# Kernel optimization log

Hardware: AMD Instinct MI355X
Metric: run time of the kernel (lower is better)

Reference implementation:

```python
import jax, jax.numpy as jnp
import numpy as np
from jax import lax

VOCAB, EMB, HID, B, T = 512, 128, 64, 256, 1024

def setup_inputs() -> dict:
    key = jax.random.key(0)
    ks = jax.random.split(key, 16)
    s = 0.1  # small init to keep tanh in its linear-ish range
    return {
        'x': jax.random.randint(ks[0], (B, T), 0, VOCAB),
        'emb': jax.random.normal(ks[1], (VOCAB, EMB), jnp.float32) * s,
        'Wih0': jax.random.normal(ks[2], (HID, EMB), jnp.float32) * s,
        'Whh0': jax.random.normal(ks[3], (HID, HID), jnp.float32) * s,
        'bih0': jax.random.normal(ks[4], (HID,), jnp.float32) * s,
        'bhh0': jax.random.normal(ks[5], (HID,), jnp.float32) * s,
        'Wih1': jax.random.normal(ks[6], (HID, HID), jnp.float32) * s,
        'Whh1': jax.random.normal(ks[7], (HID, HID), jnp.float32) * s,
        'bih1': jax.random.normal(ks[8], (HID,), jnp.float32) * s,
        'bhh1': jax.random.normal(ks[9], (HID,), jnp.float32) * s,
        'W1': jax.random.normal(ks[10], (32, HID), jnp.float32) * s,
        'b1': jax.random.normal(ks[11], (32,), jnp.float32) * s,
        'W2': jax.random.normal(ks[12], (1, 32), jnp.float32) * s,
        'b2': jax.random.normal(ks[13], (1,), jnp.float32) * s,
    }

def _rnn_layer(xs, Wih, Whh, bih, bhh):
    # xs: [T, B, D_in]; PyTorch cell: h_t = tanh(x W_ih^T + b_ih + h W_hh^T + b_hh)
    bsz = xs.shape[1]
    h0 = jnp.zeros((bsz, Whh.shape[0]), xs.dtype)
    def step(h, xt):
        h = jnp.tanh(xt @ Wih.T + bih + h @ Whh.T + bhh)
        return h, h
    hN, out = lax.scan(step, h0, xs)
    return hN, out

def reference(x, emb, Wih0, Whh0, bih0, bhh0, Wih1, Whh1, bih1, bhh1, W1, b1, W2, b2):
    xe = emb[x]                      # [B, T, EMB] embedding gather
    xs = jnp.swapaxes(xe, 0, 1)      # [T, B, EMB] time-major for scan
    _, out1 = _rnn_layer(xs, Wih0, Whh0, bih0, bhh0)   # layer 0 (dropout=0 in eval)
    hN, _ = _rnn_layer(out1, Wih1, Whh1, bih1, bhh1)   # layer 1; hN == h_n[-1]
    y = jnp.maximum(hN @ W1.T + b1, 0.0) @ W2.T + b2   # [B, 1]
    return y
```

## Files before the change

### kernel.cpp

```cpp
#include <hip/hip_runtime.h>

#define VOCAB 512
#define EMB   128
#define HID   64
#define BATCH 256
#define TLEN  1024
#define CH    16
#define NCH   (TLEN / CH)
#define RS    64
#define RCH   (RS / CH)
#define RW    96

typedef float v2f __attribute__((ext_vector_type(2)));

__device__ __forceinline__ float fast_tanh(float x) {
    float e = __expf(2.0f * x);
    return 1.0f - 2.0f / (e + 1.0f);
}
__device__ __forceinline__ void lds_fence() {
    asm volatile("s_waitcnt lgkmcnt(0)" ::: "memory");
}
__device__ __forceinline__ void compiler_fence() {
    asm volatile("" ::: "memory");
}
__device__ __forceinline__ void nap() { __builtin_amdgcn_s_sleep(1); }

__device__ __forceinline__ float dpp_xor1(float x) {
    return __int_as_float(__builtin_amdgcn_update_dpp(
        0, __float_as_int(x), 0xB1, 0xF, 0xF, false));
}
__device__ __forceinline__ float dpp_xor2(float x) {
    return __int_as_float(__builtin_amdgcn_update_dpp(
        0, __float_as_int(x), 0x4E, 0xF, 0xF, false));
}

__device__ __forceinline__ float dot_seg_rs(const float4 s[4],
                                            const v2f w[4][8],
                                            bool b0, bool b1m) {
    float p[4];
    #pragma unroll
    for (int r = 0; r < 4; ++r) {
        v2f a0 = v2f{0.f, 0.f}, a1 = v2f{0.f, 0.f};
        #pragma unroll
        for (int c = 0; c < 4; ++c) {
            float4 u = s[c];
            a0 = __builtin_elementwise_fma(v2f{u.x, u.y}, w[r][2 * c],     a0);
            a1 = __builtin_elementwise_fma(v2f{u.z, u.w}, w[r][2 * c + 1], a1);
        }
        v2f t = a0 + a1;
        p[r] = t.x + t.y;
    }
    float x01 = b0 ? p[1] : p[0];
    float y01 = b0 ? p[0] : p[1];
    x01 += dpp_xor1(y01);
    float x23 = b0 ? p[3] : p[2];
    float y23 = b0 ? p[2] : p[3];
    x23 += dpp_xor1(y23);
    float u = b1m ? x23 : x01;
    float v = b1m ? x01 : x23;
    return u + dpp_xor2(v);
}

__device__ __forceinline__ void load_w(v2f w[4][8], const float* __restrict__ W,
                                       int o, int kg) {
    #pragma unroll
    for (int r = 0; r < 4; ++r) {
        const float4* wr = (const float4*)(W + (o + 16 * r) * HID + 16 * kg);
        #pragma unroll
        for (int c = 0; c < 4; ++c) {
            float4 u = wr[c];
            w[r][2 * c]     = v2f{u.x, u.y};
            w[r][2 * c + 1] = v2f{u.z, u.w};
        }
    }
}

__device__ __forceinline__ void seg_load(float4 s[4], const float* rowkg) {
    const float4* p = (const float4*)rowkg;
    #pragma unroll
    for (int c = 0; c < 4; ++c) s[c] = p[c];
}

__global__ void __launch_bounds__(64) p0_kernel(
    const float* __restrict__ emb,
    const float* __restrict__ wih0,
    const float* __restrict__ bih0,
    const float* __restrict__ bhh0,
    float* __restrict__ P0)
{
    const int v = blockIdx.x;
    const int i = threadIdx.x;
    const float4* er = (const float4*)(emb  + v * EMB);
    const float4* wr = (const float4*)(wih0 + i * EMB);
    float a0 = 0.f, a1 = 0.f, a2 = 0.f, a3 = 0.f;
    #pragma unroll
    for (int k = 0; k < EMB / 4; ++k) {
        float4 e4 = er[k];
        float4 w4 = wr[k];
        a0 = fmaf(e4.x, w4.x, a0);
        a1 = fmaf(e4.y, w4.y, a1);
        a2 = fmaf(e4.z, w4.z, a2);
        a3 = fmaf(e4.w, w4.w, a3);
    }
    P0[v * HID + i] = (a0 + a1) + (a2 + a3) + bih0[i] + bhh0[i];
}

__global__ void __launch_bounds__(256, 1) rnn_kernel(
    const int*   __restrict__ xs,
    const float* __restrict__ P0,
    const float* __restrict__ Whh0,
    const float* __restrict__ Wih1,
    const float* __restrict__ Whh1,
    const float* __restrict__ bih1,
    const float* __restrict__ bhh1,
    const float* __restrict__ W1,
    const float* __restrict__ b1,
    const float* __restrict__ W2,
    const float* __restrict__ b2,
    float*       __restrict__ out)
{
    __shared__ float a_ring[RS][HID];
    __shared__ float h0ring[RS][RW];
    __shared__ float p1ring[RS][HID];
    __shared__ float h1buf[2][RW];
    __shared__ int   flags[4];

    const int b    = blockIdx.x;
    const int tid  = threadIdx.x;
    const int wv   = tid >> 6;
    const int lane = tid & 63;
    const int o    = lane >> 2;
    const int kg   = lane & 3;
    const int row  = o + 16 * kg;
    const int wrs  = 24 * kg + o;
    const bool b0  = (kg & 1) != 0;
    const bool b1m = (kg & 2) != 0;

    const int* xrow = xs + b * TLEN;
    const int vz = (int)__builtin_amdgcn_mbcnt_lo(0u, 0u);

    if (tid < 4) flags[tid] = 0;
    __syncthreads();

    volatile int* vf = (volatile int*)flags;

    if (wv == 0) {
        v2f w0[4][8];
        load_w(w0, Whh0, o, kg);
        __builtin_amdgcn_s_setprio(1);

        float4 s0[4];
        #pragma unroll
        for (int c = 0; c < 4; ++c) s0[c] = float4{0.f, 0.f, 0.f, 0.f};

        #pragma unroll 1
        for (int k = 0; k < NCH; ++k) {
            while (vf[3] < k + 1) nap();
            if (k >= RCH) {
                while (vf[1] < k - (RCH - 1)) nap();
            }
            compiler_fence();
            const int base = (k & (RCH - 1)) * CH;
            float a8[CH];
            #pragma unroll
            for (int i = 0; i < CH; ++i) a8[i] = a_ring[base + i][row];
            #pragma unroll
            for (int i = 0; i < CH; ++i) {
                float z  = dot_seg_rs(s0, w0, b0, b1m) + a8[i];
                float hv = fast_tanh(z);
                h0ring[base + i][wrs] = hv;
                seg_load(s0, &h0ring[base + i][24 * kg]);
            }
            lds_fence();
            if (lane == 0) vf[0] = k + 1;
        }
    } else if (wv == 1) {
        v2f wp[4][8];
        load_w(wp, Wih1, o, kg);
        const float b1s = bih1[row] + bhh1[row];

        #pragma unroll 1
        for (int k = 0; k < NCH; ++k) {
            while (vf[0] < k + 1) nap();
            if (k >= RCH) { while (vf[2] < k - (RCH - 1)) nap(); }
            compiler_fence();
            const int base = (k & (RCH - 1)) * CH;
            float4 c0[4];
            seg_load(c0, &h0ring[base][24 * kg]);
            #pragma unroll
            for (int i = 0; i < CH; ++i) {
                float4 nx[4];
                if (i < CH - 1) seg_load(nx, &h0ring[base + i + 1][24 * kg]);
                float pv = dot_seg_rs(c0, wp, b0, b1m) + b1s;
                p1ring[base + i][row] = pv;
                if (i < CH - 1) {
                    #pragma unroll
                    for (int c = 0; c < 4; ++c) c0[c] = nx[c];
                }
            }
            lds_fence();
            if (lane == 0) vf[1] = k + 1;
        }
    } else if (wv == 2) {
        v2f w2[4][8];
        load_w(w2, Whh1, o, kg);
        __builtin_amdgcn_s_setprio(1);

        float4 s1[4];
        #pragma unroll
        for (int c = 0; c < 4; ++c) s1[c] = float4{0.f, 0.f, 0.f, 0.f};

        #pragma unroll 1
        for (int k = 0; k < NCH; ++k) {
            while (vf[1] < k + 1) nap();
            compiler_fence();
            const int base = (k & (RCH - 1)) * CH;
            float p[CH];
            #pragma unroll
            for (int i = 0; i < CH; ++i) p[i] = p1ring[base + i][row];
            #pragma unroll
            for (int i = 0; i < CH; ++i) {
                const int t = k * CH + i;
                float z  = dot_seg_rs(s1, w2, b0, b1m) + p[i];
                float hv = fast_tanh(z);
                h1buf[t & 1][wrs] = hv;
                seg_load(s1, &h1buf[t & 1][24 * kg]);
            }
            lds_fence();
            if (lane == 0) vf[2] = k + 1;
        }
        __builtin_amdgcn_s_setprio(0);
        float r = 0.f;
        if (lane < 32) {
            float acc = b1[lane];
            const float* w1row = W1 + lane * HID;
            const float* hN    = h1buf[(TLEN - 1) & 1];
            #pragma unroll
            for (int j = 0; j < HID; ++j)
                acc = fmaf(w1row[j], hN[24 * (j >> 4) + (j & 15)], acc);
            r = fmaxf(acc, 0.f) * W2[lane];
        }
        #pragma unroll
        for (int off = 32; off > 0; off >>= 1) r += __shfl_down(r, off);
        if (lane == 0) out[b] = r + b2[0];
    } else {
        #pragma unroll 1
        for (int k = 0; k < NCH; ++k) {
            if (k >= RCH) {
                while (vf[0] < k - (RCH - 1)) nap();
                compiler_fence();
            }
            const int* xp = xrow + k * CH;
            int xv[CH];
            #pragma unroll
            for (int i = 0; i < CH; ++i)
                xv[i] = xp[i + vz] & (VOCAB - 1);
            float av[CH];
            #pragma unroll
            for (int i = 0; i < CH; ++i)
                av[i] = P0[xv[i] * HID + row];
            const int base = (k & (RCH - 1)) * CH;
            #pragma unroll
            for (int i = 0; i < CH; ++i)
                a_ring[base + i][row] = av[i];
            lds_fence();
            if (lane == 0) vf[3] = k + 1;
        }
    }
}

extern "C" void kernel_launch(void* const* d_in, const int* in_sizes, int n_in,
                              void* d_out, int out_size, void* d_ws, size_t ws_size,
                              hipStream_t stream)
{
    const int*   x    = (const int*)d_in[0];
    const float* emb  = (const float*)d_in[1];
    const float* Wih0 = (const float*)d_in[2];
    const float* Whh0 = (const float*)d_in[3];
    const float* bih0 = (const float*)d_in[4];
    const float* bhh0 = (const float*)d_in[5];
    const float* Wih1 = (const float*)d_in[6];
    const float* Whh1 = (const float*)d_in[7];
    const float* bih1 = (const float*)d_in[8];
    const float* bhh1 = (const float*)d_in[9];
    const float* W1   = (const float*)d_in[10];
    const float* b1   = (const float*)d_in[11];
    const float* W2   = (const float*)d_in[12];
    const float* b2   = (const float*)d_in[13];

    float* P0 = (float*)d_ws;

    hipLaunchKernelGGL(p0_kernel, dim3(VOCAB), dim3(HID), 0, stream,
                       emb, Wih0, bih0, bhh0, P0);
    hipLaunchKernelGGL(rnn_kernel, dim3(BATCH), dim3(256), 0, stream,
                       x, P0, Whh0, Wih1, Whh1, bih1, bhh1,
                       W1, b1, W2, b2, (float*)d_out);
}
```

Baseline: 286.6 us.

## Fuse both RNN layers into one skewed wavefront wave, dropping inter-wave rings

Merges the layer-0 recurrence, the layer-1 input projection and the layer-1 recurrence into a single wave. At each step that wave computes h0[t] and h1[t-1] together, sharing one small double-buffered state array. The separate h0 and p1 rings, two sync flags and two waves go away, so the block shrinks to 128 threads. This removes the cross-wave flag polling and LDS ring traffic between pipeline stages. In exchange one wave now issues three 64x64 matvec segments per step instead of one, which lengthens each serial step and raises register pressure with three resident weight sets.

```diff
diff --git a/kernel.cpp b/kernel.cpp
--- a/kernel.cpp
+++ b/kernel.cpp
@@ -34,22 +34,7 @@
         0, __float_as_int(x), 0x4E, 0xF, 0xF, false));
 }
 
-__device__ __forceinline__ float dot_seg_rs(const float4 s[4],
-                                            const v2f w[4][8],
-                                            bool b0, bool b1m) {
-    float p[4];
-    #pragma unroll
-    for (int r = 0; r < 4; ++r) {
-        v2f a0 = v2f{0.f, 0.f}, a1 = v2f{0.f, 0.f};
-        #pragma unroll
-        for (int c = 0; c < 4; ++c) {
-            float4 u = s[c];
-            a0 = __builtin_elementwise_fma(v2f{u.x, u.y}, w[r][2 * c],     a0);
-            a1 = __builtin_elementwise_fma(v2f{u.z, u.w}, w[r][2 * c + 1], a1);
-        }
-        v2f t = a0 + a1;
-        p[r] = t.x + t.y;
-    }
+__device__ __forceinline__ float quad_rs(const float p[4], bool b0, bool b1m) {
     float x01 = b0 ? p[1] : p[0];
     float y01 = b0 ? p[0] : p[1];
     x01 += dpp_xor1(y01);
@@ -59,6 +44,52 @@
     float u = b1m ? x23 : x01;
     float v = b1m ? x01 : x23;
     return u + dpp_xor2(v);
+}
+
+__device__ __forceinline__ float dot_seg_rs(const float4 s[4],
+                                            const v2f w[4][8],
+                                            bool b0, bool b1m) {
+    float p[4];
+    #pragma unroll
+    for (int r = 0; r < 4; ++r) {
+        v2f a0 = v2f{0.f, 0.f}, a1 = v2f{0.f, 0.f};
+        #pragma unroll
+        for (int c = 0; c < 4; ++c) {
+            float4 u = s[c];
+            a0 = __builtin_elementwise_fma(v2f{u.x, u.y}, w[r][2 * c],     a0);
+            a1 = __builtin_elementwise_fma(v2f{u.z, u.w}, w[r][2 * c + 1], a1);
+        }
+        v2f t = a0 + a1;
+        p[r] = t.x + t.y;
+    }
+    return quad_rs(p, b0, b1m);
+}
+
+__device__ __forceinline__ float dot2_seg_rs(const float4 s0[4],
+                                             const v2f wB[4][8],
+                                             const float4 s1[4],
+                                             const v2f wC[4][8],
+                                             bool b0, bool b1m) {
+    float p[4];
+    #pragma unroll
+    for (int r = 0; r < 4; ++r) {
+        v2f a0 = v2f{0.f, 0.f}, a1 = v2f{0.f, 0.f};
+        #pragma unroll
+        for (int c = 0; c < 4; ++c) {
+            float4 u = s0[c];
+            a0 = __builtin_elementwise_fma(v2f{u.x, u.y}, wB[r][2 * c],     a0);
+            a1 = __builtin_elementwise_fma(v2f{u.z, u.w}, wB[r][2 * c + 1], a1);
+        }
+        #pragma unroll
+        for (int c = 0; c < 4; ++c) {
+            float4 u = s1[c];
+            a0 = __builtin_elementwise_fma(v2f{u.x, u.y}, wC[r][2 * c],     a0);
+            a1 = __builtin_elementwise_fma(v2f{u.z, u.w}, wC[r][2 * c + 1], a1);
+        }
+        v2f t = a0 + a1;
+        p[r] = t.x + t.y;
+    }
+    return quad_rs(p, b0, b1m);
 }
 
 __device__ __forceinline__ void load_w(v2f w[4][8], const float* __restrict__ W,
@@ -105,7 +136,7 @@
     P0[v * HID + i] = (a0 + a1) + (a2 + a3) + bih0[i] + bhh0[i];
 }
 
-__global__ void __launch_bounds__(256, 1) rnn_kernel(
+__global__ void __launch_bounds__(128, 1) rnn_kernel(
     const int*   __restrict__ xs,
     const float* __restrict__ P0,
     const float* __restrict__ Whh0,
@@ -120,10 +151,8 @@
     float*       __restrict__ out)
 {
     __shared__ float a_ring[RS][HID];
-    __shared__ float h0ring[RS][RW];
-    __shared__ float p1ring[RS][HID];
-    __shared__ float h1buf[2][RW];
-    __shared__ int   flags[4];
+    __shared__ float sring[2][2][RW];
+    __shared__ int   flags[2];
 
     const int b    = blockIdx.x;
     const int tid  = threadIdx.x;
@@ -139,102 +168,58 @@
     const int* xrow = xs + b * TLEN;
     const int vz = (int)__builtin_amdgcn_mbcnt_lo(0u, 0u);
 
-    if (tid < 4) flags[tid] = 0;
+    if (tid < 2) flags[tid] = 0;
     __syncthreads();
 
     volatile int* vf = (volatile int*)flags;
 
     if (wv == 0) {
-        v2f w0[4][8];
-        load_w(w0, Whh0, o, kg);
+        v2f wA[4][8], wB[4][8], wC[4][8];
+        load_w(wA, Whh0, o, kg);
+        load_w(wB, Wih1, o, kg);
+        load_w(wC, Whh1, o, kg);
+        const float b1s = bih1[row] + bhh1[row];
         __builtin_amdgcn_s_setprio(1);
 
-        float4 s0[4];
-        #pragma unroll
-        for (int c = 0; c < 4; ++c) s0[c] = float4{0.f, 0.f, 0.f, 0.f};
-
-        #pragma unroll 1
-        for (int k = 0; k < NCH; ++k) {
-            while (vf[3] < k + 1) nap();
-            if (k >= RCH) {
-                while (vf[1] < k - (RCH - 1)) nap();
-            }
-            compiler_fence();
-            const int base = (k & (RCH - 1)) * CH;
-            float a8[CH];
-            #pragma unroll
-            for (int i = 0; i < CH; ++i) a8[i] = a_ring[base + i][row];
-            #pragma unroll
-            for (int i = 0; i < CH; ++i) {
-                float z  = dot_seg_rs(s0, w0, b0, b1m) + a8[i];
-                float hv = fast_tanh(z);
-                h0ring[base + i][wrs] = hv;
-                seg_load(s0, &h0ring[base + i][24 * kg]);
-            }
-            lds_fence();
-            if (lane == 0) vf[0] = k + 1;
-        }
-    } else if (wv == 1) {
-        v2f wp[4][8];
-        load_w(wp, Wih1, o, kg);
-        const float b1s = bih1[row] + bhh1[row];
-
-        #pragma unroll 1
-        for (int k = 0; k < NCH; ++k) {
-            while (vf[0] < k + 1) nap();
-            if (k >= RCH) { while (vf[2] < k - (RCH - 1)) nap(); }
-            compiler_fence();
-            const int base = (k & (RCH - 1)) * CH;
-            float4 c0[4];
-            seg_load(c0, &h0ring[base][24 * kg]);
-            #pragma unroll
-            for (int i = 0; i < CH; ++i) {
-                float4 nx[4];
-                if (i < CH - 1) seg_load(nx, &h0ring[base + i + 1][24 * kg]);
-                float pv = dot_seg_rs(c0, wp, b0, b1m) + b1s;
-                p1ring[base + i][row] = pv;
-                if (i < CH - 1) {
-                    #pragma unroll
-                    for (int c = 0; c < 4; ++c) c0[c] = nx[c];
-                }
-            }
-            lds_fence();
-            if (lane == 0) vf[1] = k + 1;
-        }
-    } else if (wv == 2) {
-        v2f w2[4][8];
-        load_w(w2, Whh1, o, kg);
-        __builtin_amdgcn_s_setprio(1);
-
-        float4 s1[4];
-        #pragma unroll
-        for (int c = 0; c < 4; ++c) s1[c] = float4{0.f, 0.f, 0.f, 0.f};
+        float4 sh0[4], sh1[4];
+        #pragma unroll
+        for (int c = 0; c < 4; ++c) {
+            sh0[c] = float4{0.f, 0.f, 0.f, 0.f};
+            sh1[c] = float4{0.f, 0.f, 0.f, 0.f};
+        }
 
         #pragma unroll 1
         for (int k = 0; k < NCH; ++k) {
             while (vf[1] < k + 1) nap();
             compiler_fence();
             const int base = (k & (RCH - 1)) * CH;
-            float p[CH];
-            #pragma unroll
-            for (int i = 0; i < CH; ++i) p[i] = p1ring[base + i][row];
+            float a8[CH];
+            #pragma unroll
+            for (int i = 0; i < CH; ++i) a8[i] = a_ring[base + i][row];
             #pragma unroll
             for (int i = 0; i < CH; ++i) {
                 const int t = k * CH + i;
-                float z  = dot_seg_rs(s1, w2, b0, b1m) + p[i];
-                float hv = fast_tanh(z);
-                h1buf[t & 1][wrs] = hv;
-                seg_load(s1, &h1buf[t & 1][24 * kg]);
+                float zA = dot_seg_rs(sh0, wA, b0, b1m) + a8[i];
+                float zH = dot2_seg_rs(sh0, wB, sh1, wC, b0, b1m) + b1s;
+                float h0v = fast_tanh(zA);
+                float h1v = (t == 0) ? 0.f : fast_tanh(zH);
+                sring[t & 1][0][wrs] = h0v;
+                sring[t & 1][1][wrs] = h1v;
+                seg_load(sh0, &sring[t & 1][0][24 * kg]);
+                seg_load(sh1, &sring[t & 1][1][24 * kg]);
             }
             lds_fence();
-            if (lane == 0) vf[2] = k + 1;
-        }
-        __builtin_amdgcn_s_setprio(0);
+            if (lane == 0) vf[0] = k + 1;
+        }
+        float zH = dot2_seg_rs(sh0, wB, sh1, wC, b0, b1m) + b1s;
+        float h1f = fast_tanh(zH);
+        sring[0][1][wrs] = h1f;
+        lds_fence();
         float r = 0.f;
         if (lane < 32) {
             float acc = b1[lane];
             const float* w1row = W1 + lane * HID;
-            const float* hN    = h1buf[(TLEN - 1) & 1];
+            const float* hN    = sring[0][1];
             #pragma unroll
             for (int j = 0; j < HID; ++j)
                 acc = fmaf(w1row[j], hN[24 * (j >> 4) + (j & 15)], acc);
@@ -264,7 +249,7 @@
             for (int i = 0; i < CH; ++i)
                 a_ring[base + i][row] = av[i];
             lds_fence();
-            if (lane == 0) vf[3] = k + 1;
+            if (lane == 0) vf[1] = k + 1;
         }
     }
 }
@@ -292,7 +277,7 @@
 
     hipLaunchKernelGGL(p0_kernel, dim3(VOCAB), dim3(HID), 0, stream,
                        emb, Wih0, bih0, bhh0, P0);
-    hipLaunchKernelGGL(rnn_kernel, dim3(BATCH), dim3(256), 0, stream,
+    hipLaunchKernelGGL(rnn_kernel, dim3(BATCH), dim3(128), 0, stream,
                        x, P0, Whh0, Wih1, Whh1, bih1, bhh1,
                        W1, b1, W2, b2, (float*)d_out);
 }
```

Measured after the change: 459.7 us. 60.4% more time.
